# Kernel tuning notes

Hardware: AMD Instinct MI355X
Metric: run time of the kernel (lower is better)

## Reference

```python
import jax, jax.numpy as jnp
import numpy as np

B, N, K, DIM, NB, RES, PAD = 2, 8192, 16, 64, 5, 64, 0.1
H = DIM // 2  # bottleneck width of FKABlock
PLANES = ((0, 1), (0, 2), (1, 2))  # xy, xz, yz


def setup_inputs() -> dict:
    key = jax.random.key(0)
    ks = jax.random.split(key, 10)
    xyz = jax.random.uniform(ks[0], (B, N, 3), jnp.float32) - 0.5

    def w(k, shape, fan_in):
        return jax.random.normal(k, shape, jnp.float32) / np.sqrt(fan_in)

    return {
        "xyz": xyz,
        "w_stem": w(ks[1], (3, DIM), 3),
        "b_stem": jnp.zeros((DIM,), jnp.float32),
        "w0": w(ks[2], (NB, DIM, H), DIM),
        "b0": jnp.zeros((NB, H), jnp.float32),
        "fc1": w(ks[3], (NB, 3, K), 3),
        "fc2": w(ks[4], (NB, 2 * K, K), 2 * K),
        "fc3": w(ks[5], (NB, 2 * K, K), 2 * K),
        "wcv": w(ks[6], (NB, H, H, K), H * K),
        "alpha": jnp.ones((NB,), jnp.float32),
        "beta": jnp.ones((NB,), jnp.float32),
        "w2": w(ks[7], (NB, H, DIM), H),
        "b2": jnp.zeros((NB, DIM), jnp.float32),
    }


def _knn_idx(xyz, k):
    # brute-force squared distances (b, n, n); top-k smallest -> neighbor indices
    sq = jnp.sum(xyz * xyz, -1)
    d2 = sq[:, :, None] + sq[:, None, :] - 2.0 * jnp.einsum('bnd,bmd->bnm', xyz, xyz)
    _, idx = jax.lax.top_k(-d2, k)
    return idx  # (b, n, k) int32


_gather = jax.vmap(lambda f, i: f[i])  # (n, c), (n, k) -> (n, k, c), vmapped over batch


def _fkaconv(x, xyz, idx, fc1, fc2, fc3, wcv, alpha, beta):
    nb_pos = _gather(xyz, idx)                 # (b, n, k, 3)
    pts = nb_pos - xyz[:, :, None, :]          # local coordinates
    # distances are detached in the original (pts.detach())
    dists = jnp.sqrt(jnp.sum(jax.lax.stop_gradient(pts) ** 2, -1) + 1e-12)  # (b, n, k)
    dw = jax.nn.sigmoid(-alpha * dists + beta)
    dw = dw / (jnp.sum(dw, -1, keepdims=True) + 1e-6) * K
    dwe = dw[..., None]                        # (b, n, k, 1)
    # kernel-weight estimation MLP with masked max-pool over neighbors
    m = jax.nn.relu(pts @ fc1)                 # (b, n, k, K)
    mp = jnp.max(m * dwe, 2, keepdims=True)
    m = jax.nn.relu(jnp.concatenate([m, jnp.broadcast_to(mp, m.shape)], -1) @ fc2)
    mp = jnp.max(m * dwe, 2, keepdims=True)
    m = jax.nn.relu(jnp.concatenate([m, jnp.broadcast_to(mp, m.shape)], -1) @ fc3)
    m = m * dwe                                # (b, n, k, K)
    nb_x = _gather(x, idx)                     # (b, n, k, h)
    # f[b,n,c,s] = sum_k nb_x * m ; out[b,n,o] = sum_{c,s} f * wcv[o,c,s]
    return jnp.einsum('bnkc,bnks,ocs->bno', nb_x, m, wcv)


def _triplane(c, xyz):
    pn = xyz / (1.0 + PAD + 1e-3) + 0.5        # normalize to [0, 1]
    ij = jnp.clip((pn * RES).astype(jnp.int32), 0, RES - 1)  # (b, n, 3)
    bidx = jnp.arange(B, dtype=jnp.int32)[:, None]
    cf = c.reshape(B * N, DIM)
    ones = jnp.ones((B * N,), c.dtype)
    planes = []
    for a, b2 in PLANES:
        seg = (bidx * (RES * RES) + ij[..., a] * RES + ij[..., b2]).reshape(-1)
        s = jax.ops.segment_sum(cf, seg, num_segments=B * RES * RES)
        cnt = jax.ops.segment_sum(ones, seg, num_segments=B * RES * RES)
        planes.append((s / jnp.maximum(cnt, 1.0)[:, None]).reshape(B, RES, RES, DIM))
    return jnp.stack(planes, 1)                # (b, 3, res, res, dim)


def reference(xyz, w_stem, b_stem, w0, b0, fc1, fc2, fc3, wcv, alpha, beta, w2, b2):
    c = xyz @ w_stem + b_stem                  # stem linear
    idx = _knn_idx(xyz, K)                     # knn_points(xyz, xyz, K)
    for i in range(NB):                        # FKABlock residual blocks
        x = jax.nn.relu(c @ w0[i] + b0[i])
        x = jax.nn.relu(_fkaconv(x, xyz, idx, fc1[i], fc2[i], fc3[i], wcv[i], alpha[i], beta[i]))
        x = x @ w2[i] + b2[i]
        c = jax.nn.relu(x + c)
    tri_feat = _triplane(c, xyz)
    return (xyz, c, tri_feat)
```

## Files before the change

### kernel.cpp

```cpp
#include <hip/hip_runtime.h>
#include <math.h>

#define BB 2
#define NN 8192
#define KK 16
#define DIMM 64
#define HH 32
#define NBB 5
#define RESS 64
#define NPTS (BB*NN)
#define PLANE_ELEMS (BB*3*RESS*RESS*DIMM)
#define PLANE_CELLS (BB*3*RESS*RESS)
#define GC 8
#define GCS 0.125f
#define NCELL (GC*GC*GC)
#define CAP 640
#define GRP 3

__global__ void zero_kernel(float* __restrict__ p, int n) {
  int t = blockIdx.x * blockDim.x + threadIdx.x;
  if (t < n) p[t] = 0.0f;
}

__global__ void stem_kernel(const float* __restrict__ xyz,
                            const float* __restrict__ w,
                            const float* __restrict__ bias,
                            float* __restrict__ out_xyz,
                            float* __restrict__ c) {
  int tid = blockIdx.x * blockDim.x + threadIdx.x;
  if (tid < NPTS*3) out_xyz[tid] = xyz[tid];
  if (tid < NPTS*DIMM) {
    int p = tid >> 6, d = tid & 63;
    float x = xyz[p*3+0], y = xyz[p*3+1], z = xyz[p*3+2];
    c[tid] = x*w[d] + y*w[64+d] + z*w[128+d] + bias[d];
  }
}

__device__ __forceinline__ unsigned ord32(float f) {
  unsigned u = __float_as_uint(f);
  return u ^ ((unsigned)((int)u >> 31) | 0x80000000u);
}
__device__ __forceinline__ int cell_of(float v) {
  return min(max((int)((v + 0.5f) * 8.0f), 0), 7);
}

__global__ void knn_count_kernel(const float* __restrict__ xyz,
                                 int* __restrict__ cellcnt) {
  int p = blockIdx.x * blockDim.x + threadIdx.x;
  if (p >= NPTS) return;
  int bq = p >> 13;
  float px = xyz[p*3], py = xyz[p*3+1], pz = xyz[p*3+2];
  int cc = (cell_of(px) << 6) | (cell_of(py) << 3) | cell_of(pz);
  atomicAdd(&cellcnt[(bq << 9) | cc], 1);
}

__global__ __launch_bounds__(1024) void knn_scan_kernel(const int* __restrict__ cnt,
                                                        int* __restrict__ cellstart,
                                                        int* __restrict__ cellcur) {
  __shared__ int s[1024];
  int t = threadIdx.x;
  int v = cnt[t];
  s[t] = v;
  __syncthreads();
  for (int off = 1; off < 1024; off <<= 1) {
    int add = (t >= off) ? s[t-off] : 0;
    __syncthreads();
    s[t] += add;
    __syncthreads();
  }
  int inc = s[t];
  cellstart[t+1] = inc;
  if (t == 0) cellstart[0] = 0;
  cellcur[t] = inc - v;
}

__global__ void knn_scatter_kernel(const float* __restrict__ xyz,
                                   int* __restrict__ cellcur,
                                   float4* __restrict__ spts) {
  int p = blockIdx.x * blockDim.x + threadIdx.x;
  if (p >= NPTS) return;
  int bq = p >> 13;
  float px = xyz[p*3], py = xyz[p*3+1], pz = xyz[p*3+2];
  int cc = (cell_of(px) << 6) | (cell_of(py) << 3) | cell_of(pz);
  int pos = atomicAdd(&cellcur[(bq << 9) | cc], 1);
  spts[pos] = make_float4(px, py, pz, __int_as_float(p & (NN-1)));
}

#define U64MIN(a,b) (((a) < (b)) ? (a) : (b))
#define U64MAX(a,b) (((a) < (b)) ? (b) : (a))

#define INS64(key)                                                             \
  {                                                                            \
    unsigned long long _k = (key);                                             \
    _Pragma("unroll")                                                          \
    for (int jj = 15; jj >= 1; --jj) {                                         \
      unsigned long long up = bd[jj-1];                                        \
      bool shift = _k < up;                                                    \
      bool here  = _k < bd[jj];                                                \
      unsigned long long nv = shift ? up : _k;                                 \
      bd[jj] = here ? nv : bd[jj];                                             \
    }                                                                          \
    bd[0] = (_k < bd[0]) ? _k : bd[0];                                         \
  }

#define DRAIN64()                                                              \
  {                                                                            \
    INS64((0 < fcnt) ? fd[0] : ~0ull);                                         \
    INS64((1 < fcnt) ? fd[1] : ~0ull);                                         \
    INS64((2 < fcnt) ? fd[2] : ~0ull);                                         \
    INS64((3 < fcnt) ? fd[3] : ~0ull);                                         \
    fcnt = 0; hi15 = (unsigned)(bd[15] >> 32);                                 \
  }

#define TRYKEY_F(c4)                                                           \
  {                                                                            \
    float sq = (c4).x*(c4).x + (c4).y*(c4).y + (c4).z*(c4).z;                  \
    float d2 = (qs + sq) - 2.0f*(qx*(c4).x + qy*(c4).y + qz*(c4).z);           \
    unsigned du = ord32(d2);                                                   \
    bool hit = valid && du <= hi15;                                            \
    unsigned long long key =                                                   \
        ((unsigned long long)du << 32) | (unsigned)__float_as_int((c4).w);     \
    _Pragma("unroll")                                                          \
    for (int j2 = 0; j2 < 4; ++j2)                                             \
      fd[j2] = (hit && fcnt == j2) ? key : fd[j2];                             \
    fcnt += hit;                                                               \
    if (__any(fcnt >= 4)) { DRAIN64(); }                                       \
  }

#define TRYKEY(c4)                                                             \
  {                                                                            \
    float sq = (c4).x*(c4).x + (c4).y*(c4).y + (c4).z*(c4).z;                  \
    float d2 = (qs + sq) - 2.0f*(qx*(c4).x + qy*(c4).y + qz*(c4).z);           \
    unsigned du = ord32(d2);                                                   \
    bool hit = valid && du <= hi15;                                            \
    if (__any(hit)) {                                                          \
      unsigned long long key = hit ?                                           \
          (((unsigned long long)du << 32) | (unsigned)__float_as_int((c4).w))  \
          : ~0ull;                                                             \
      INS64(key);                                                              \
      hi15 = (unsigned)(bd[15] >> 32);                                         \
    }                                                                          \
  }

#define BMERGE_STEP(MASK)                                                      \
  {                                                                            \
    unsigned long long tmp[16];                                                \
    _Pragma("unroll")                                                          \
    for (int j = 0; j < 16; ++j) tmp[j] = __shfl_xor(bd[15-j], MASK);          \
    _Pragma("unroll")                                                          \
    for (int j = 0; j < 16; ++j) bd[j] = U64MIN(bd[j], tmp[j]);                \
    _Pragma("unroll")                                                          \
    for (int dd2 = 8; dd2 >= 1; dd2 >>= 1) {                                   \
      _Pragma("unroll")                                                        \
      for (int i2 = 0; i2 < 16; ++i2) {                                        \
        if ((i2 & dd2) == 0) {                                                 \
          unsigned long long a2 = bd[i2], b2 = bd[i2 + dd2];                   \
          bd[i2] = U64MIN(a2, b2); bd[i2 + dd2] = U64MAX(a2, b2);              \
        }                                                                      \
      }                                                                        \
    }                                                                          \
    hi15 = (unsigned)(bd[15] >> 32);                                           \
  }

#define MERGE_STEP(MASK)                                                       \
  {                                                                            \
    unsigned long long tmp[16];                                                \
    _Pragma("unroll")                                                          \
    for (int j = 0; j < 16; ++j) tmp[j] = __shfl_xor(bd[j], MASK);             \
    _Pragma("unroll")                                                          \
    for (int j = 0; j < 16; ++j) {                                             \
      unsigned long long _in = tmp[j];                                         \
      bool dup = false;                                                        \
      _Pragma("unroll")                                                        \
      for (int jj = 0; jj < 16; ++jj) dup = dup || (bd[jj] == _in);            \
      INS64(dup ? ~0ull : _in);                                                \
    }                                                                          \
    hi15 = (unsigned)(bd[15] >> 32);                                           \
  }

__global__ __launch_bounds__(64) void knn_query_kernel(
    const float4* __restrict__ spts, const int* __restrict__ cellstart,
    int* __restrict__ idx) {
  __shared__ __align__(16) float4 s_cand[CAP];
  __shared__ int s_ofs[28];
  __shared__ int s_jlo[27];
  int wave = blockIdx.x / GRP;
  int g = blockIdx.x % GRP;
  int b = wave >> 9;
  int cell = wave & 511;
  int cx = cell >> 6, cy = (cell >> 3) & 7, cz = cell & 7;
  int cb = b << 9;
  int qlo = cellstart[cb + cell], qhi = cellstart[cb + cell + 1];
  int nq = qhi - qlo;
  if (nq <= 0 || 16*g >= nq) return;
  int lane = threadIdx.x;
  int q = lane & 15, s = lane >> 4;

  int x0 = max(cx-1,0), x1 = min(cx+1,7);
  int y0 = max(cy-1,0), y1 = min(cy+1,7);
  int z0 = max(cz-1,0), z1 = min(cz+1,7);
  int dy = y1-y0+1, dz = z1-z0+1;
  int count = (x1-x0+1)*dy*dz;
  int len = 0, jlo0 = 0;
  if (lane < count) {
    int xx = x0 + lane/(dy*dz);
    int rem = lane % (dy*dz);
    int yy = y0 + rem/dz, zz = z0 + rem % dz;
    int cc = cb + (xx<<6) + (yy<<3) + zz;
    jlo0 = cellstart[cc];
    len = cellstart[cc+1] - jlo0;
  }
  int pre = len;
#pragma unroll
  for (int off = 1; off < 64; off <<= 1) {
    int v = __shfl_up(pre, off);
    if (lane >= off) pre += v;
  }
  if (lane < count) { s_ofs[lane] = pre - len; s_jlo[lane] = jlo0; }
  if (lane == count-1) s_ofs[count] = pre;
  __syncthreads();
  int total = s_ofs[count];
  int tstag = min(total, CAP);

  for (int w = lane; w < tstag; w += 64) {
    int lo2 = 0, hi2 = count-1;
    while (lo2 < hi2) { int mid = (lo2+hi2+1)>>1; if (s_ofs[mid] <= w) lo2 = mid; else hi2 = mid-1; }
    s_cand[w] = spts[s_jlo[lo2] + (w - s_ofs[lo2])];
  }
  __syncthreads();

  const unsigned thru1 = ord32((GCS - 1e-4f)*(GCS - 1e-4f));
  for (int qg = 16*g; qg < nq; qg += 16*GRP) {
    bool valid = (qg + q) < nq;
    float4 qv = spts[qlo + qg + (valid ? q : 0)];
    float qx = qv.x, qy = qv.y, qz = qv.z;
    float qs = qx*qx + qy*qy + qz*qz;
    unsigned long long bd[16];
#pragma unroll
    for (int j = 0; j < 16; ++j) bd[j] = ~0ull;
    unsigned long long fd[4] = {0,0,0,0};
    int fcnt = 0;
    unsigned hi15 = 0xFFFFFFFFu;

    int chunk = (tstag + 3) >> 2;
    int jb = s*chunk, je = min(jb+chunk, tstag);
    for (int j = jb; j < je; ++j) {
      float4 c4 = s_cand[j];
      TRYKEY_F(c4);
    }
    if (__any(fcnt > 0)) { DRAIN64(); }
    if (total > CAP) {
      for (int i = 0; i < count; ++i) {
        int ofs_i = s_ofs[i], len_i = s_ofs[i+1]-ofs_i;
        int stg = min(max(CAP - ofs_i, 0), len_i);
        int jl = s_jlo[i] + stg, jh = s_jlo[i] + len_i;
        for (int j2 = jl + s; j2 < jh; j2 += 4) {
          float4 c4 = spts[j2];
          TRYKEY(c4);
        }
      }
    }
    BMERGE_STEP(16);
    BMERGE_STEP(32);
    bool done = !valid || (hi15 < thru1);
    for (int r = 2; r <= 8; ++r) {
      if (!__any(!done)) break;
      int xs0 = max(cx-r,0), xs1 = min(cx+r,7);
      int ys0 = max(cy-r,0), ys1 = min(cy+r,7);
      int zs0 = max(cz-r,0), zs1 = min(cz+r,7);
      int pr = r-1;
      for (int xx = xs0; xx <= xs1; ++xx)
      for (int yy = ys0; yy <= ys1; ++yy)
      for (int zz = zs0; zz <= zs1; ++zz) {
        if (xx >= cx-pr && xx <= cx+pr && yy >= cy-pr && yy <= cy+pr &&
            zz >= cz-pr && zz <= cz+pr) continue;
        int cc2 = cb + (xx<<6) + (yy<<3) + zz;
        int jl = cellstart[cc2], jh = cellstart[cc2+1];
        for (int j2 = jl + s; j2 < jh; j2 += 4) {
          float4 c4 = spts[j2];
          TRYKEY(c4);
        }
      }
      MERGE_STEP(16);
      MERGE_STEP(32);
      float thr2 = (float)r * GCS - 1e-4f;
      done = !valid || (hi15 < ord32(thr2*thr2));
    }
    if (valid && s == 0) {
      int n_self = __float_as_int(qv.w);
      int* op = idx + (((long)b << 13) + n_self) * 16;
#pragma unroll
      for (int j = 0; j < 16; ++j) op[j] = (int)(unsigned)(bd[j] & 0xffffffffu);
    }
  }
}

__global__ void xproj_kernel(const float* __restrict__ c,
                             const float* __restrict__ w0,
                             const float* __restrict__ b0,
                             float* __restrict__ x, int layer) {
  int tid = blockIdx.x * blockDim.x + threadIdx.x;
  if (tid >= NPTS*HH) return;
  int p = tid >> 5, h = tid & 31;
  const float* w = w0 + layer*DIMM*HH;
  const float* cr = c + p*DIMM;
  float acc = b0[layer*HH + h];
#pragma unroll
  for (int d = 0; d < DIMM; ++d) acc += cr[d]*w[d*HH + h];
  x[tid] = fmaxf(acc, 0.0f);
}

#define OFF_W1   0
#define OFF_W2AT 48
#define OFF_W2BT 368
#define OFF_W3AT 688
#define OFF_W3BT 1008
#define OFF_B2   1328
#define OFF_RED  1392
#define OFF_Y    2416
#define OFF_SCR  2544
#define SCR_SZ   1296
#define S_DW 0
#define S_M1 16
#define S_M2 272
#define S_MM 528
#define S_XN 784
#define S_FB 16
#define LDS_TOT (OFF_SCR + 4*SCR_SZ)

__global__ __launch_bounds__(256) void conv_kernel(
    float* __restrict__ c, const float* __restrict__ x,
    const int* __restrict__ idx, const float* __restrict__ xyz,
    const float* __restrict__ fc1, const float* __restrict__ fc2,
    const float* __restrict__ fc3, const float* __restrict__ wcv,
    const float* __restrict__ alpha, const float* __restrict__ beta,
    const float* __restrict__ w2, const float* __restrict__ b2, int layer)
{
  __shared__ __align__(16) float lds[LDS_TOT];
  int t = threadIdx.x;

  const float* fc1l = fc1 + layer*3*KK;
  const float* fc2l = fc2 + layer*2*KK*KK;
  const float* fc3l = fc3 + layer*2*KK*KK;
  const float* wcvl = wcv + layer*HH*HH*KK;
  const float* w2l  = w2  + layer*HH*DIMM;
  const float* b2l  = b2  + layer*DIMM;

  if (t < 48) lds[OFF_W1 + t] = fc1l[t];
  {
    int s = t >> 4, tt = t & 15;
    lds[OFF_W2AT + s*20 + tt] = fc2l[tt*16 + s];
    lds[OFF_W2BT + s*20 + tt] = fc2l[(16+tt)*16 + s];
    lds[OFF_W3AT + s*20 + tt] = fc3l[tt*16 + s];
    lds[OFF_W3BT + s*20 + tt] = fc3l[(16+tt)*16 + s];
  }
  if (t < 64) lds[OFF_B2 + t] = b2l[t];
  __syncthreads();

  int wv = t >> 6, lane = t & 63;
  int p = blockIdx.x*4 + wv;
  int b = p >> 13;
  float* scr = lds + OFF_SCR + wv*SCR_SZ;
  int sI = lane & 15;

  float qxx = xyz[p*3+0], qyy = xyz[p*3+1], qzz = xyz[p*3+2];
  float alv = alpha[layer], bev = beta[layer];
  int jidx = 0; float px = 0, py = 0, pz = 0, sv = 0;
  if (lane < 16) {
    jidx = idx[p*16 + lane];
    const float* nb = xyz + ((long)b*NN + jidx)*3;
    px = nb[0]-qxx; py = nb[1]-qyy; pz = nb[2]-qzz;
    float dd = sqrtf(px*px + py*py + pz*pz + 1e-12f);
    sv = 1.0f/(1.0f + expf(alv*dd - bev));
  }
  float ssum = 0.0f;
#pragma unroll
  for (int k = 0; k < 16; ++k) ssum += __shfl(sv, k);
  if (lane < 16) scr[S_DW + lane] = sv / (ssum + 1e-6f) * 16.0f;
#pragma unroll
  for (int r = 0; r < 2; ++r) {
    int tsk = lane + 64*r;
    int k = tsk >> 3, seg = tsk & 7;
    int jk = __shfl(jidx, k);
    float4 v = *(const float4*)(x + ((long)b*NN + jk)*32 + seg*4);
    *(float4*)&scr[S_XN + k*32 + seg*4] = v;
  }
#pragma unroll
  for (int r = 0; r < 4; ++r) {
    int k = (lane >> 4) + 4*r;
    float pxk = __shfl(px, k), pyk = __shfl(py, k), pzk = __shfl(pz, k);
    float v = pxk*lds[OFF_W1+sI] + pyk*lds[OFF_W1+16+sI] + pzk*lds[OFF_W1+32+sI];
    scr[S_M1 + k*16 + sI] = fmaxf(v, 0.0f);
  }

  {
    float mpv = 0.0f;
#pragma unroll
    for (int k = 0; k < 16; ++k) mpv = fmaxf(mpv, scr[S_M1 + k*16 + sI] * scr[S_DW + k]);
    float qv = 0.0f;
#pragma unroll
    for (int tt = 0; tt < 16; ++tt) qv += __shfl(mpv, tt) * lds[OFF_W2BT + sI*20 + tt];
    float4 wa0 = *(float4*)&lds[OFF_W2AT + sI*20 + 0];
    float4 wa1 = *(float4*)&lds[OFF_W2AT + sI*20 + 4];
    float4 wa2 = *(float4*)&lds[OFF_W2AT + sI*20 + 8];
    float4 wa3 = *(float4*)&lds[OFF_W2AT + sI*20 + 12];
#pragma unroll
    for (int r = 0; r < 4; ++r) {
      int k = (lane >> 4) + 4*r;
      float4 m0 = *(float4*)&scr[S_M1 + k*16 + 0];
      float4 m1_ = *(float4*)&scr[S_M1 + k*16 + 4];
      float4 m2_ = *(float4*)&scr[S_M1 + k*16 + 8];
      float4 m3_ = *(float4*)&scr[S_M1 + k*16 + 12];
      float v = qv;
      v += m0.x*wa0.x; v += m0.y*wa0.y; v += m0.z*wa0.z; v += m0.w*wa0.w;
      v += m1_.x*wa1.x; v += m1_.y*wa1.y; v += m1_.z*wa1.z; v += m1_.w*wa1.w;
      v += m2_.x*wa2.x; v += m2_.y*wa2.y; v += m2_.z*wa2.z; v += m2_.w*wa2.w;
      v += m3_.x*wa3.x; v += m3_.y*wa3.y; v += m3_.z*wa3.z; v += m3_.w*wa3.w;
      scr[S_M2 + k*16 + sI] = fmaxf(v, 0.0f);
    }
  }

  {
    float mpv = 0.0f;
#pragma unroll
    for (int k = 0; k < 16; ++k) mpv = fmaxf(mpv, scr[S_M2 + k*16 + sI] * scr[S_DW + k]);
    float qv = 0.0f;
#pragma unroll
    for (int tt = 0; tt < 16; ++tt) qv += __shfl(mpv, tt) * lds[OFF_W3BT + sI*20 + tt];
    float4 wa0 = *(float4*)&lds[OFF_W3AT + sI*20 + 0];
    float4 wa1 = *(float4*)&lds[OFF_W3AT + sI*20 + 4];
    float4 wa2 = *(float4*)&lds[OFF_W3AT + sI*20 + 8];
    float4 wa3 = *(float4*)&lds[OFF_W3AT + sI*20 + 12];
#pragma unroll
    for (int r = 0; r < 4; ++r) {
      int k = (lane >> 4) + 4*r;
      float4 m0 = *(float4*)&scr[S_M2 + k*16 + 0];
      float4 m1_ = *(float4*)&scr[S_M2 + k*16 + 4];
      float4 m2_ = *(float4*)&scr[S_M2 + k*16 + 8];
      float4 m3_ = *(float4*)&scr[S_M2 + k*16 + 12];
      float v = qv;
      v += m0.x*wa0.x; v += m0.y*wa0.y; v += m0.z*wa0.z; v += m0.w*wa0.w;
      v += m1_.x*wa1.x; v += m1_.y*wa1.y; v += m1_.z*wa1.z; v += m1_.w*wa1.w;
      v += m2_.x*wa2.x; v += m2_.y*wa2.y; v += m2_.z*wa2.z; v += m2_.w*wa2.w;
      v += m3_.x*wa3.x; v += m3_.y*wa3.y; v += m3_.z*wa3.z; v += m3_.w*wa3.w;
      scr[S_MM + k*16 + sI] = fmaxf(v, 0.0f) * scr[S_DW + k];
    }
  }

  {
    int q4 = lane >> 4;
    float fr0=0,fr1=0,fr2=0,fr3=0,fr4=0,fr5=0,fr6=0,fr7=0;
#pragma unroll
    for (int k = 0; k < 16; ++k) {
      float mmv = scr[S_MM + k*16 + sI];
      float4 a  = *(float4*)&scr[S_XN + k*32 + q4*8];
      float4 bb = *(float4*)&scr[S_XN + k*32 + q4*8 + 4];
      fr0 += a.x*mmv;  fr1 += a.y*mmv;  fr2 += a.z*mmv;  fr3 += a.w*mmv;
      fr4 += bb.x*mmv; fr5 += bb.y*mmv; fr6 += bb.z*mmv; fr7 += bb.w*mmv;
    }
    scr[S_FB + (q4*8+0)*16 + sI] = fr0;
    scr[S_FB + (q4*8+1)*16 + sI] = fr1;
    scr[S_FB + (q4*8+2)*16 + sI] = fr2;
    scr[S_FB + (q4*8+3)*16 + sI] = fr3;
    scr[S_FB + (q4*8+4)*16 + sI] = fr4;
    scr[S_FB + (q4*8+5)*16 + sI] = fr5;
    scr[S_FB + (q4*8+6)*16 + sI] = fr6;
    scr[S_FB + (q4*8+7)*16 + sI] = fr7;
  }
  __syncthreads();

  {
    int o = t & 31, seg = t >> 5;
    const float4* wrow = (const float4*)(wcvl + o*512 + seg*64);
    float acc0=0, acc1=0, acc2=0, acc3=0;
#pragma unroll
    for (int j = 0; j < 16; ++j) {
      float4 w4 = wrow[j];
      float4 f0 = *(const float4*)&lds[OFF_SCR + 0*SCR_SZ + S_FB + seg*64 + j*4];
      float4 f1 = *(const float4*)&lds[OFF_SCR + 1*SCR_SZ + S_FB + seg*64 + j*4];
      float4 f2 = *(const float4*)&lds[OFF_SCR + 2*SCR_SZ + S_FB + seg*64 + j*4];
      float4 f3 = *(const float4*)&lds[OFF_SCR + 3*SCR_SZ + S_FB + seg*64 + j*4];
      acc0 += w4.x*f0.x; acc0 += w4.y*f0.y; acc0 += w4.z*f0.z; acc0 += w4.w*f0.w;
      acc1 += w4.x*f1.x; acc1 += w4.y*f1.y; acc1 += w4.z*f1.z; acc1 += w4.w*f1.w;
      acc2 += w4.x*f2.x; acc2 += w4.y*f2.y; acc2 += w4.z*f2.z; acc2 += w4.w*f2.w;
      acc3 += w4.x*f3.x; acc3 += w4.y*f3.y; acc3 += w4.z*f3.z; acc3 += w4.w*f3.w;
    }
    lds[OFF_RED + seg*128 + 0*32 + o] = acc0;
    lds[OFF_RED + seg*128 + 1*32 + o] = acc1;
    lds[OFF_RED + seg*128 + 2*32 + o] = acc2;
    lds[OFF_RED + seg*128 + 3*32 + o] = acc3;
  }
  __syncthreads();

  if (t < 128) {
    int pt = t >> 5, o = t & 31;
    float yv = 0.0f;
#pragma unroll
    for (int seg = 0; seg < 8; ++seg) yv += lds[OFF_RED + seg*128 + pt*32 + o];
    lds[OFF_Y + pt*32 + o] = fmaxf(yv, 0.0f);
  }
  __syncthreads();

  {
    int pt = t >> 6, d = t & 63;
    float zv = lds[OFF_B2 + d];
    const float* w2g = w2l + d;
#pragma unroll
    for (int o = 0; o < 32; ++o) zv += lds[OFF_Y + pt*32 + o] * w2g[o*64];
    int gp = blockIdx.x*4 + pt;
    float cv = c[gp*64 + d];
    c[gp*64 + d] = fmaxf(zv + cv, 0.0f);
  }
}

__global__ void triacc_kernel(const float* __restrict__ c,
                              const float* __restrict__ xyz,
                              float* __restrict__ psum,
                              float* __restrict__ pcnt) {
  int tid = blockIdx.x * blockDim.x + threadIdx.x;
  if (tid >= NPTS*DIMM) return;
  int p = tid >> 6, d = tid & 63;
  int b = p >> 13;
  float p0 = xyz[p*3+0] / 1.101f + 0.5f;
  float p1 = xyz[p*3+1] / 1.101f + 0.5f;
  float p2 = xyz[p*3+2] / 1.101f + 0.5f;
  int i0 = min(max((int)(p0*64.0f), 0), 63);
  int i1 = min(max((int)(p1*64.0f), 0), 63);
  int i2 = min(max((int)(p2*64.0f), 0), 63);
  int cb = b*3*RESS*RESS;
  int c0 = cb + 0*RESS*RESS + i0*RESS + i1;
  int c1 = cb + 1*RESS*RESS + i0*RESS + i2;
  int c2 = cb + 2*RESS*RESS + i1*RESS + i2;
  float v = c[tid];
  atomicAdd(&psum[c0*DIMM + d], v);
  atomicAdd(&psum[c1*DIMM + d], v);
  atomicAdd(&psum[c2*DIMM + d], v);
  if (d == 0) {
    atomicAdd(&pcnt[c0], 1.0f);
    atomicAdd(&pcnt[c1], 1.0f);
    atomicAdd(&pcnt[c2], 1.0f);
  }
}

__global__ void trinorm_kernel(const float* __restrict__ psum,
                               const float* __restrict__ pcnt,
                               float* __restrict__ out) {
  int tid = blockIdx.x * blockDim.x + threadIdx.x;
  if (tid >= PLANE_ELEMS) return;
  float cnt = pcnt[tid >> 6];
  out[tid] = psum[tid] / fmaxf(cnt, 1.0f);
}

extern "C" void kernel_launch(void* const* d_in, const int* in_sizes, int n_in,
                              void* d_out, int out_size, void* d_ws, size_t ws_size,
                              hipStream_t stream) {
  const float* xyz   = (const float*)d_in[0];
  const float* wstem = (const float*)d_in[1];
  const float* bstem = (const float*)d_in[2];
  const float* w0    = (const float*)d_in[3];
  const float* b0    = (const float*)d_in[4];
  const float* fc1   = (const float*)d_in[5];
  const float* fc2   = (const float*)d_in[6];
  const float* fc3   = (const float*)d_in[7];
  const float* wcv   = (const float*)d_in[8];
  const float* alpha = (const float*)d_in[9];
  const float* beta  = (const float*)d_in[10];
  const float* w2    = (const float*)d_in[11];
  const float* b2    = (const float*)d_in[12];

  float* out     = (float*)d_out;
  float* out_xyz = out;
  float* c       = out + NPTS*3;
  float* out_tri = c + NPTS*DIMM;

  float* wsf  = (float*)d_ws;
  int*   idx  = (int*)d_ws;
  float* x    = wsf + NPTS*16;
  float* psum = x + NPTS*HH;
  float* pcnt = psum + PLANE_ELEMS;

  int*    cellcnt   = (int*)psum;
  int*    cellstart = (int*)psum + 1024;
  int*    cellcur   = (int*)psum + 2056;
  float4* spts      = (float4*)(psum + 4096);

  stem_kernel<<<(NPTS*DIMM+255)/256, 256, 0, stream>>>(xyz, wstem, bstem, out_xyz, c);
  zero_kernel<<<4, 256, 0, stream>>>((float*)cellcnt, 1024);
  knn_count_kernel<<<(NPTS+255)/256, 256, 0, stream>>>(xyz, cellcnt);
  knn_scan_kernel<<<1, 1024, 0, stream>>>(cellcnt, cellstart, cellcur);
  knn_scatter_kernel<<<(NPTS+255)/256, 256, 0, stream>>>(xyz, cellcur, spts);
  knn_query_kernel<<<1024*GRP, 64, 0, stream>>>(spts, cellstart, idx);
  for (int layer = 0; layer < NBB; ++layer) {
    xproj_kernel<<<(NPTS*HH+255)/256, 256, 0, stream>>>(c, w0, b0, x, layer);
    conv_kernel<<<NPTS/4, 256, 0, stream>>>(c, x, idx, xyz, fc1, fc2, fc3, wcv,
                                            alpha, beta, w2, b2, layer);
  }
  int nz = PLANE_ELEMS + PLANE_CELLS;
  zero_kernel<<<(nz+255)/256, 256, 0, stream>>>(psum, nz);
  triacc_kernel<<<(NPTS*DIMM+255)/256, 256, 0, stream>>>(c, xyz, psum, pcnt);
  trinorm_kernel<<<(PLANE_ELEMS+255)/256, 256, 0, stream>>>(psum, pcnt, out_tri);
}
```

Measured before the change: 540.6 us.

## Fuse next-layer input projection into conv epilogue and stem

Removes the per-layer xproj kernel. Each conv block now computes the next layer's bottleneck projection from its freshly updated c rows held in LDS, writing into ping-pong x buffers. Layer 0's projection and the kNN cell counting are folded into the stem kernel, which cuts launches and re-reads of c. The cost is extra LDS, an extra barrier per conv block, and redundant stem recomputation (64 FMAs of c per x element) in the stem kernel.

```diff
diff --git a/kernel.cpp b/kernel.cpp
--- a/kernel.cpp
+++ b/kernel.cpp
@@ -22,36 +22,47 @@
   if (t < n) p[t] = 0.0f;
 }
 
+__device__ __forceinline__ int cell_of(float v) {
+  return min(max((int)((v + 0.5f) * 8.0f), 0), 7);
+}
+
 __global__ void stem_kernel(const float* __restrict__ xyz,
                             const float* __restrict__ w,
                             const float* __restrict__ bias,
+                            const float* __restrict__ w0,
+                            const float* __restrict__ b0,
                             float* __restrict__ out_xyz,
-                            float* __restrict__ c) {
+                            float* __restrict__ c,
+                            float* __restrict__ x0,
+                            int* __restrict__ cellcnt) {
   int tid = blockIdx.x * blockDim.x + threadIdx.x;
   if (tid < NPTS*3) out_xyz[tid] = xyz[tid];
   if (tid < NPTS*DIMM) {
     int p = tid >> 6, d = tid & 63;
     float x = xyz[p*3+0], y = xyz[p*3+1], z = xyz[p*3+2];
     c[tid] = x*w[d] + y*w[64+d] + z*w[128+d] + bias[d];
+    if (d == 0) {
+      int bq = p >> 13;
+      int cc = (cell_of(x) << 6) | (cell_of(y) << 3) | cell_of(z);
+      atomicAdd(&cellcnt[(bq << 9) | cc], 1);
+    }
+  }
+  if (tid < NPTS*HH) {
+    int p = tid >> 5, h = tid & 31;
+    float x = xyz[p*3+0], y = xyz[p*3+1], z = xyz[p*3+2];
+    float acc = b0[h];
+#pragma unroll
+    for (int d = 0; d < DIMM; ++d) {
+      float cd = x*w[d] + y*w[64+d] + z*w[128+d] + bias[d];
+      acc += cd * w0[d*HH + h];
+    }
+    x0[tid] = fmaxf(acc, 0.0f);
   }
 }
 
 __device__ __forceinline__ unsigned ord32(float f) {
   unsigned u = __float_as_uint(f);
   return u ^ ((unsigned)((int)u >> 31) | 0x80000000u);
-}
-__device__ __forceinline__ int cell_of(float v) {
-  return min(max((int)((v + 0.5f) * 8.0f), 0), 7);
-}
-
-__global__ void knn_count_kernel(const float* __restrict__ xyz,
-                                 int* __restrict__ cellcnt) {
-  int p = blockIdx.x * blockDim.x + threadIdx.x;
-  if (p >= NPTS) return;
-  int bq = p >> 13;
-  float px = xyz[p*3], py = xyz[p*3+1], pz = xyz[p*3+2];
-  int cc = (cell_of(px) << 6) | (cell_of(py) << 3) | cell_of(pz);
-  atomicAdd(&cellcnt[(bq << 9) | cc], 1);
 }
 
 __global__ __launch_bounds__(1024) void knn_scan_kernel(const int* __restrict__ cnt,
@@ -295,21 +306,6 @@
   }
 }
 
-__global__ void xproj_kernel(const float* __restrict__ c,
-                             const float* __restrict__ w0,
-                             const float* __restrict__ b0,
-                             float* __restrict__ x, int layer) {
-  int tid = blockIdx.x * blockDim.x + threadIdx.x;
-  if (tid >= NPTS*HH) return;
-  int p = tid >> 5, h = tid & 31;
-  const float* w = w0 + layer*DIMM*HH;
-  const float* cr = c + p*DIMM;
-  float acc = b0[layer*HH + h];
-#pragma unroll
-  for (int d = 0; d < DIMM; ++d) acc += cr[d]*w[d*HH + h];
-  x[tid] = fmaxf(acc, 0.0f);
-}
-
 #define OFF_W1   0
 #define OFF_W2AT 48
 #define OFF_W2BT 368
@@ -318,7 +314,8 @@
 #define OFF_B2   1328
 #define OFF_RED  1392
 #define OFF_Y    2416
-#define OFF_SCR  2544
+#define OFF_CN   2544
+#define OFF_SCR  2800
 #define SCR_SZ   1296
 #define S_DW 0
 #define S_M1 16
@@ -329,12 +326,14 @@
 #define LDS_TOT (OFF_SCR + 4*SCR_SZ)
 
 __global__ __launch_bounds__(256) void conv_kernel(
-    float* __restrict__ c, const float* __restrict__ x,
+    float* __restrict__ c, const float* __restrict__ xin,
+    float* __restrict__ xout,
     const int* __restrict__ idx, const float* __restrict__ xyz,
     const float* __restrict__ fc1, const float* __restrict__ fc2,
     const float* __restrict__ fc3, const float* __restrict__ wcv,
     const float* __restrict__ alpha, const float* __restrict__ beta,
-    const float* __restrict__ w2, const float* __restrict__ b2, int layer)
+    const float* __restrict__ w2, const float* __restrict__ b2,
+    const float* __restrict__ w0, const float* __restrict__ b0, int layer)
 {
   __shared__ __align__(16) float lds[LDS_TOT];
   int t = threadIdx.x;
@@ -345,6 +344,9 @@
   const float* wcvl = wcv + layer*HH*HH*KK;
   const float* w2l  = w2  + layer*HH*DIMM;
   const float* b2l  = b2  + layer*DIMM;
+  bool do_x = (layer + 1) < NBB;
+  const float* w0n = w0 + (layer+1)*DIMM*HH;
+  const float* b0n = b0 + (layer+1)*HH;
 
   if (t < 48) lds[OFF_W1 + t] = fc1l[t];
   {
@@ -382,7 +384,7 @@
     int tsk = lane + 64*r;
     int k = tsk >> 3, seg = tsk & 7;
     int jk = __shfl(jidx, k);
-    float4 v = *(const float4*)(x + ((long)b*NN + jk)*32 + seg*4);
+    float4 v = *(const float4*)(xin + ((long)b*NN + jk)*32 + seg*4);
     *(float4*)&scr[S_XN + k*32 + seg*4] = v;
   }
 #pragma unroll
@@ -509,7 +511,20 @@
     for (int o = 0; o < 32; ++o) zv += lds[OFF_Y + pt*32 + o] * w2g[o*64];
     int gp = blockIdx.x*4 + pt;
     float cv = c[gp*64 + d];
-    c[gp*64 + d] = fmaxf(zv + cv, 0.0f);
+    float cnew = fmaxf(zv + cv, 0.0f);
+    c[gp*64 + d] = cnew;
+    lds[OFF_CN + pt*64 + d] = cnew;
+  }
+  if (do_x) {
+    __syncthreads();
+    if (t < 128) {
+      int pt = t >> 5, h = t & 31;
+      float acc = b0n[h];
+#pragma unroll
+      for (int d = 0; d < DIMM; ++d) acc += lds[OFF_CN + pt*64 + d] * w0n[d*HH + h];
+      int gp = blockIdx.x*4 + pt;
+      xout[gp*HH + h] = fmaxf(acc, 0.0f);
+    }
   }
 }
 
@@ -575,25 +590,28 @@
 
   float* wsf  = (float*)d_ws;
   int*   idx  = (int*)d_ws;
-  float* x    = wsf + NPTS*16;
-  float* psum = x + NPTS*HH;
+  float* xA   = wsf + NPTS*16;
+  float* psum = xA + NPTS*HH;
   float* pcnt = psum + PLANE_ELEMS;
 
   int*    cellcnt   = (int*)psum;
   int*    cellstart = (int*)psum + 1024;
   int*    cellcur   = (int*)psum + 2056;
   float4* spts      = (float4*)(psum + 4096);
-
-  stem_kernel<<<(NPTS*DIMM+255)/256, 256, 0, stream>>>(xyz, wstem, bstem, out_xyz, c);
+  float*  xB        = psum + 69632;
+
   zero_kernel<<<4, 256, 0, stream>>>((float*)cellcnt, 1024);
-  knn_count_kernel<<<(NPTS+255)/256, 256, 0, stream>>>(xyz, cellcnt);
+  stem_kernel<<<(NPTS*DIMM+255)/256, 256, 0, stream>>>(
+      xyz, wstem, bstem, w0, b0, out_xyz, c, xA, cellcnt);
   knn_scan_kernel<<<1, 1024, 0, stream>>>(cellcnt, cellstart, cellcur);
   knn_scatter_kernel<<<(NPTS+255)/256, 256, 0, stream>>>(xyz, cellcur, spts);
   knn_query_kernel<<<1024*GRP, 64, 0, stream>>>(spts, cellstart, idx);
   for (int layer = 0; layer < NBB; ++layer) {
-    xproj_kernel<<<(NPTS*HH+255)/256, 256, 0, stream>>>(c, w0, b0, x, layer);
-    conv_kernel<<<NPTS/4, 256, 0, stream>>>(c, x, idx, xyz, fc1, fc2, fc3, wcv,
-                                            alpha, beta, w2, b2, layer);
+    float* xin  = (layer & 1) ? xB : xA;
+    float* xout = (layer & 1) ? xA : xB;
+    conv_kernel<<<NPTS/4, 256, 0, stream>>>(c, xin, xout, idx, xyz,
+                                            fc1, fc2, fc3, wcv, alpha, beta,
+                                            w2, b2, w0, b0, layer);
   }
   int nz = PLANE_ELEMS + PLANE_CELLS;
   zero_kernel<<<(nz+255)/256, 256, 0, stream>>>(psum, nz);
```

Result: faster. 502.0 us (-7.1%).
